# Performance work log

Measured on AMD Instinct MI355X. Metric: run time of the kernel, lower is better.

## Reference

```python
import jax, jax.numpy as jnp
import numpy as np

N_NODES = 50000
ALPHA_SLOPE = 0.2  # LeakyReLU negative slope
EPS = 1e-16


def setup_inputs() -> dict:
    key = jax.random.key(0)
    k1, k2, k3, k4 = jax.random.split(key, 4)
    in_features, heads, d = 512, 8, 32
    x = jax.random.normal(k1, (N_NODES, in_features), dtype=jnp.float32)
    edge_index = jax.random.randint(k2, (2, 800000), 0, N_NODES, dtype=jnp.int64)
    # xavier_normal with relu gain ~ sqrt(2) * sqrt(2/(fan_in+fan_out))
    w_std = np.sqrt(2.0) * np.sqrt(2.0 / (in_features + d))
    a_std = np.sqrt(2.0) * np.sqrt(2.0 / (1 + 2 * d))
    W = jax.random.normal(k3, (heads, in_features, d), dtype=jnp.float32) * w_std
    a = jax.random.normal(k4, (heads, 2 * d), dtype=jnp.float32) * a_std
    return {"x": x, "edge_index": edge_index, "W": W, "a": a}


def reference(x, edge_index, W, a):
    # x: [N, F_in], edge_index: [2, E], W: [H, F_in, D], a: [H, 2D]
    n = x.shape[0]
    d = W.shape[-1]
    e0, e1 = edge_index[0], edge_index[1]
    # per-head projected features: [N, H, D]
    h = jnp.einsum('nf,hfd->nhd', x, W)
    # attention logits: a.mm(cat(h[e0], h[e1]).T) == a_src.h[e0] + a_dst.h[e1]
    a_src, a_dst = a[:, :d], a[:, d:]          # [H, D] each
    s_src = jnp.einsum('nhd,hd->nh', h, a_src)  # [N, H]
    s_dst = jnp.einsum('nhd,hd->nh', h, a_dst)  # [N, H]
    logits = s_src[e0] + s_dst[e1]              # [E, H]
    logits = jnp.where(logits >= 0, logits, ALPHA_SLOPE * logits)  # LeakyReLU
    # segment softmax over destination node e0
    m = jax.ops.segment_max(logits, e0, num_segments=n)   # [N, H]
    ex = jnp.exp(logits - m[e0])                          # [E, H]
    denom = jax.ops.segment_sum(ex, e0, num_segments=n)   # [N, H]
    alpha = ex / (denom[e0] + EPS)                        # [E, H]
    # dropout is identity in eval mode
    # sparse aggregate: out[e0] += alpha * h[e1]
    msg = alpha[:, :, None] * h[e1]                       # [E, H, D]
    out = jax.ops.segment_sum(msg, e0, num_segments=n)    # [N, H, D]
    return out.reshape(n, -1)                             # concat heads -> [N, H*D]
```

## Files before the change

### kernel.cpp

```cpp
#include <hip/hip_runtime.h>

#define N_NODES 50000
#define N_EDGES 800000
#define IN_F    512
#define HEADS   8
#define DHEAD   32
#define NHD     256
#define SLOPE   0.2f
#define EPS_F   1e-16f
#define N_SBLK  ((N_NODES + 255) / 256)

typedef __attribute__((ext_vector_type(8))) short short8;
typedef __attribute__((ext_vector_type(4))) float f32x4;
typedef __attribute__((ext_vector_type(4))) unsigned short u16x4;

__device__ __forceinline__ unsigned short f2bf(float f) {
  unsigned int u = __float_as_uint(f);
  unsigned int r = u + 0x7FFFu + ((u >> 16) & 1u);
  return (unsigned short)(r >> 16);
}
__device__ __forceinline__ float bf2f(unsigned short s) {
  return __uint_as_float(((unsigned int)s) << 16);
}
__device__ __forceinline__ void gload_lds16(const void* g, void* l) {
  __builtin_amdgcn_global_load_lds((const __attribute__((address_space(1))) void*)g,
                                   (__attribute__((address_space(3))) void*)l, 16, 0, 0);
}

__global__ void k_cast_w(const float* __restrict__ W, unsigned short* __restrict__ WbT) {
  int id = blockIdx.x * blockDim.x + threadIdx.x;
  if (id >= NHD * IN_F) return;
  int c = id >> 9, k = id & 511;
  WbT[id] = f2bf(W[(c >> 5) * (IN_F * DHEAD) + k * DHEAD + (c & 31)]);
}

__global__ __launch_bounds__(256) void k_gemm_mfma(const float* __restrict__ x,
                                                   const unsigned short* __restrict__ WbT,
                                                   unsigned short* __restrict__ hb) {
  __shared__ unsigned short As[64 * 64];
  __shared__ unsigned short Bs[256 * 64];
  const int tid  = threadIdx.x;
  const int lane = tid & 63;
  const int wid  = tid >> 6;
  const int bm   = blockIdx.x * 64;
  const int wn   = wid * 64;

  const int arow = tid >> 3, ap = tid & 7, aq = ap ^ (arow & 7);
  const float* gA0 = x + (size_t)min(bm + arow,      N_NODES - 1) * IN_F + aq * 8;
  const float* gA1 = x + (size_t)min(bm + arow + 32, N_NODES - 1) * IN_F + aq * 8;
  unsigned short* lA0 = &As[(arow * 8 + ap) * 8];
  unsigned short* lA1 = &As[((arow + 32) * 8 + ap) * 8];

  const int bs = 512 * wid + lane;
  const int brow = bs >> 3, bp = bs & 7, bq = bp ^ (brow & 7);
  const unsigned short* gB = WbT + (size_t)brow * IN_F + bq * 8;
  unsigned short* lB = &Bs[(size_t)512 * wid * 8];

  f32x4 acc[4][4] = {};

  for (int k0 = 0; k0 < IN_F; k0 += 64) {
    __syncthreads();
#pragma unroll
    for (int it = 0; it < 8; ++it)
      gload_lds16(gB + k0 + it * 8 * IN_F, lB + it * 64 * 8);
    {
      float4 a00 = *(const float4*)(gA0 + k0);
      float4 a01 = *(const float4*)(gA0 + k0 + 4);
      float4 a10 = *(const float4*)(gA1 + k0);
      float4 a11 = *(const float4*)(gA1 + k0 + 4);
      short8 v0, v1;
      v0[0] = (short)f2bf(a00.x); v0[1] = (short)f2bf(a00.y);
      v0[2] = (short)f2bf(a00.z); v0[3] = (short)f2bf(a00.w);
      v0[4] = (short)f2bf(a01.x); v0[5] = (short)f2bf(a01.y);
      v0[6] = (short)f2bf(a01.z); v0[7] = (short)f2bf(a01.w);
      v1[0] = (short)f2bf(a10.x); v1[1] = (short)f2bf(a10.y);
      v1[2] = (short)f2bf(a10.z); v1[3] = (short)f2bf(a10.w);
      v1[4] = (short)f2bf(a11.x); v1[5] = (short)f2bf(a11.y);
      v1[6] = (short)f2bf(a11.z); v1[7] = (short)f2bf(a11.w);
      *(short8*)lA0 = v0;
      *(short8*)lA1 = v1;
    }
    __syncthreads();

#pragma unroll
    for (int kk = 0; kk < 2; ++kk) {
      short8 af[4], bfr[4];
#pragma unroll
      for (int i = 0; i < 4; ++i) {
        int r = i * 16 + (lane & 15);
        int q = kk * 4 + (lane >> 4);
        af[i] = *(const short8*)&As[(r * 8 + (q ^ (r & 7))) * 8];
      }
#pragma unroll
      for (int j = 0; j < 4; ++j) {
        int r = wn + j * 16 + (lane & 15);
        int q = kk * 4 + (lane >> 4);
        bfr[j] = *(const short8*)&Bs[(r * 8 + (q ^ (r & 7))) * 8];
      }
#pragma unroll
      for (int i = 0; i < 4; ++i)
#pragma unroll
        for (int j = 0; j < 4; ++j)
          acc[i][j] = __builtin_amdgcn_mfma_f32_16x16x32_bf16(af[i], bfr[j], acc[i][j], 0, 0, 0);
    }
  }

#pragma unroll
  for (int i = 0; i < 4; ++i) {
#pragma unroll
    for (int q = 0; q < 4; ++q) {
      int row = bm + i * 16 + (lane >> 4) * 4 + q;
      if (row < N_NODES) {
#pragma unroll
        for (int j = 0; j < 4; ++j)
          hb[(size_t)row * NHD + wn + j * 16 + (lane & 15)] = f2bf(acc[i][j][q]);
      }
    }
  }
}

__global__ __launch_bounds__(256) void k_scores(const unsigned short* __restrict__ hb,
                                                const float* __restrict__ a,
                                                float* __restrict__ s_src,
                                                float* __restrict__ s_dst) {
  int n = (blockIdx.x * blockDim.x + threadIdx.x) >> 6;
  int lane = threadIdx.x & 63;
  if (n >= N_NODES) return;
  int head = lane >> 3;
  int dofs = (lane & 7) * 4;
  u16x4 hv = *(const u16x4*)(hb + (size_t)n * NHD + lane * 4);
  float4 as = *(const float4*)(a + head * 2 * DHEAD + dofs);
  float4 ad = *(const float4*)(a + head * 2 * DHEAD + DHEAD + dofs);
  float h0 = bf2f(hv.x), h1 = bf2f(hv.y), h2 = bf2f(hv.z), h3 = bf2f(hv.w);
  float ss = h0 * as.x + h1 * as.y + h2 * as.z + h3 * as.w;
  float sd = h0 * ad.x + h1 * ad.y + h2 * ad.z + h3 * ad.w;
  ss += __shfl_xor(ss, 1); ss += __shfl_xor(ss, 2); ss += __shfl_xor(ss, 4);
  sd += __shfl_xor(sd, 1); sd += __shfl_xor(sd, 2); sd += __shfl_xor(sd, 4);
  if ((lane & 7) == 0) {
    s_src[n * 8 + head] = ss;
    s_dst[n * 8 + head] = sd;
  }
}

__global__ void k_hist(const int* __restrict__ ei, int* __restrict__ deg) {
  int e = blockIdx.x * blockDim.x + threadIdx.x;
  if (e < N_EDGES) atomicAdd(&deg[ei[e]], 1);
}

__global__ __launch_bounds__(256) void k_bsum(const int* __restrict__ deg,
                                              int* __restrict__ bsum) {
  __shared__ int sm[4];
  int i = blockIdx.x * 256 + threadIdx.x;
  int v = (i < N_NODES) ? deg[i] : 0;
#pragma unroll
  for (int o = 1; o < 64; o <<= 1) v += __shfl_xor(v, o);
  if ((threadIdx.x & 63) == 0) sm[threadIdx.x >> 6] = v;
  __syncthreads();
  if (threadIdx.x == 0) bsum[blockIdx.x] = sm[0] + sm[1] + sm[2] + sm[3];
}

__global__ __launch_bounds__(256) void k_scan_main(const int* __restrict__ deg,
                                                   const int* __restrict__ bsum,
                                                   int* __restrict__ rowptr,
                                                   int* __restrict__ cursor) {
  __shared__ int sb[256];
  __shared__ int sm[256];
  const int t = threadIdx.x;
  const int b = blockIdx.x;
  int bv = (t < N_SBLK) ? bsum[t] : 0;
  sb[t] = bv;
  int i = b * 256 + t;
  int v = (i < N_NODES) ? deg[i] : 0;
  sm[t] = v;
  __syncthreads();
#pragma unroll
  for (int o = 1; o < 256; o <<= 1) {
    int u1 = (t >= o) ? sb[t - o] : 0;
    int u2 = (t >= o) ? sm[t - o] : 0;
    __syncthreads();
    sb[t] += u1;
    sm[t] += u2;
    __syncthreads();
  }
  int boff = (b > 0) ? sb[b - 1] : 0;
  if (i < N_NODES) {
    int ex = boff + sm[t] - v;
    rowptr[i] = ex;
    cursor[i] = ex;
  }
  if (b == 0 && t == 0) rowptr[N_NODES] = sb[255];
}

__global__ void k_fill(const int* __restrict__ ei, int* __restrict__ cursor,
                       int* __restrict__ edst) {
  int e = blockIdx.x * blockDim.x + threadIdx.x;
  if (e >= N_EDGES) return;
  int p = atomicAdd(&cursor[ei[e]], 1);
  edst[p] = ei[N_EDGES + e];
}

__global__ __launch_bounds__(256) void k_aggr(const int* __restrict__ rowptr,
                                              const int* __restrict__ edst,
                                              const float* __restrict__ s_src,
                                              const float* __restrict__ s_dst,
                                              const unsigned short* __restrict__ hb,
                                              float* __restrict__ out) {
  int n = (int)((blockIdx.x * blockDim.x + threadIdx.x) >> 6);
  if (n >= N_NODES) return;
  n = __builtin_amdgcn_readfirstlane(n);
  const int lane = threadIdx.x & 63;
  const int head = lane >> 3;
  const float ssrc = s_src[n * 8 + head];
  int i = rowptr[n];
  const int iend = rowptr[n + 1];
  float den = 0.f;
  f32x4 acc = {0.f, 0.f, 0.f, 0.f};
  for (; i + 1 < iend; i += 2) {
    int d0 = edst[i], d1 = edst[i + 1];
    float v0 = ssrc + s_dst[d0 * 8 + head];
    float v1 = ssrc + s_dst[d1 * 8 + head];
    u16x4 h0 = *(const u16x4*)(hb + (size_t)d0 * NHD + lane * 4);
    u16x4 h1 = *(const u16x4*)(hb + (size_t)d1 * NHD + lane * 4);
    v0 = v0 >= 0.f ? v0 : SLOPE * v0;
    v1 = v1 >= 0.f ? v1 : SLOPE * v1;
    float e0 = __expf(v0), e1 = __expf(v1);
    den += e0 + e1;
    acc.x += e0 * bf2f(h0.x) + e1 * bf2f(h1.x);
    acc.y += e0 * bf2f(h0.y) + e1 * bf2f(h1.y);
    acc.z += e0 * bf2f(h0.z) + e1 * bf2f(h1.z);
    acc.w += e0 * bf2f(h0.w) + e1 * bf2f(h1.w);
  }
  if (i < iend) {
    int d0 = edst[i];
    float v0 = ssrc + s_dst[d0 * 8 + head];
    v0 = v0 >= 0.f ? v0 : SLOPE * v0;
    float e0 = __expf(v0);
    u16x4 h0 = *(const u16x4*)(hb + (size_t)d0 * NHD + lane * 4);
    den += e0;
    acc.x += e0 * bf2f(h0.x);
    acc.y += e0 * bf2f(h0.y);
    acc.z += e0 * bf2f(h0.z);
    acc.w += e0 * bf2f(h0.w);
  }
  float inv = 1.f / (den + EPS_F);
  *(f32x4*)(out + (size_t)n * NHD + lane * 4) = acc * inv;
}

extern "C" void kernel_launch(void* const* d_in, const int* in_sizes, int n_in,
                              void* d_out, int out_size, void* d_ws, size_t ws_size,
                              hipStream_t stream) {
  const float* x  = (const float*)d_in[0];
  const int*   ei = (const int*)d_in[1];
  const float* W  = (const float*)d_in[2];
  const float* a  = (const float*)d_in[3];
  float* out = (float*)d_out;

  unsigned short* hb  = (unsigned short*)d_ws;
  unsigned short* WbT = hb + (size_t)N_NODES * NHD;
  float* s_src = (float*)(WbT + (size_t)NHD * IN_F);
  float* s_dst = s_src + (size_t)N_NODES * HEADS;
  int* deg    = (int*)(s_dst + (size_t)N_NODES * HEADS);
  int* cursor = deg + N_NODES;
  int* rowptr = cursor + N_NODES;
  int* bsum   = rowptr + 50008;
  int* edst   = bsum + 256;

  hipMemsetAsync(deg, 0, (size_t)N_NODES * sizeof(int), stream);
  k_cast_w<<<(NHD * IN_F + 255) / 256, 256, 0, stream>>>(W, WbT);
  k_gemm_mfma<<<(N_NODES + 63) / 64, 256, 0, stream>>>(x, WbT, hb);
  k_scores<<<(N_NODES * 64 + 255) / 256, 256, 0, stream>>>(hb, a, s_src, s_dst);
  k_hist<<<(N_EDGES + 255) / 256, 256, 0, stream>>>(ei, deg);
  k_bsum<<<N_SBLK, 256, 0, stream>>>(deg, bsum);
  k_scan_main<<<N_SBLK, 256, 0, stream>>>(deg, bsum, rowptr, cursor);
  k_fill<<<(N_EDGES + 255) / 256, 256, 0, stream>>>(ei, cursor, edst);
  k_aggr<<<(N_NODES * 64 + 255) / 256, 256, 0, stream>>>(rowptr, edst, s_src, s_dst, hb, out);
}
```

Measured before the change: 204.2 us.

## Fuse score computation into GEMM, double-buffer GEMM, merge prep kernels, unroll aggregation

Attention-score dot products move into the GEMM epilogue using accumulator registers plus shuffle reductions, so the separate scores kernel and its re-read of h are removed. The GEMM gains double-buffered LDS for A and B so global loads overlap MFMA work. The weight cast and degree histogram are combined into one launch, and the aggregation loop is unrolled by four to keep more gathers in flight. LDS use per block doubles, which may lower occupancy.

```diff
diff --git a/kernel.cpp b/kernel.cpp
--- a/kernel.cpp
+++ b/kernel.cpp
@@ -27,18 +27,26 @@
                                    (__attribute__((address_space(3))) void*)l, 16, 0, 0);
 }
 
-__global__ void k_cast_w(const float* __restrict__ W, unsigned short* __restrict__ WbT) {
-  int id = blockIdx.x * blockDim.x + threadIdx.x;
-  if (id >= NHD * IN_F) return;
-  int c = id >> 9, k = id & 511;
-  WbT[id] = f2bf(W[(c >> 5) * (IN_F * DHEAD) + k * DHEAD + (c & 31)]);
+__global__ __launch_bounds__(256) void k_prep(const float* __restrict__ W,
+                                              unsigned short* __restrict__ WbT,
+                                              const int* __restrict__ ei,
+                                              int* __restrict__ deg) {
+  int id = blockIdx.x * 256 + threadIdx.x;
+  if (id < NHD * IN_F) {
+    int c = id >> 9, k = id & 511;
+    WbT[id] = f2bf(W[(c >> 5) * (IN_F * DHEAD) + k * DHEAD + (c & 31)]);
+  }
+  if (id < N_EDGES) atomicAdd(&deg[ei[id]], 1);
 }
 
 __global__ __launch_bounds__(256) void k_gemm_mfma(const float* __restrict__ x,
                                                    const unsigned short* __restrict__ WbT,
-                                                   unsigned short* __restrict__ hb) {
-  __shared__ unsigned short As[64 * 64];
-  __shared__ unsigned short Bs[256 * 64];
+                                                   unsigned short* __restrict__ hb,
+                                                   const float* __restrict__ a,
+                                                   float* __restrict__ s_src,
+                                                   float* __restrict__ s_dst) {
+  __shared__ unsigned short As[2][64 * 64];
+  __shared__ unsigned short Bs[2][256 * 64];
   const int tid  = threadIdx.x;
   const int lane = tid & 63;
   const int wid  = tid >> 6;
@@ -48,40 +56,39 @@
   const int arow = tid >> 3, ap = tid & 7, aq = ap ^ (arow & 7);
   const float* gA0 = x + (size_t)min(bm + arow,      N_NODES - 1) * IN_F + aq * 8;
   const float* gA1 = x + (size_t)min(bm + arow + 32, N_NODES - 1) * IN_F + aq * 8;
-  unsigned short* lA0 = &As[(arow * 8 + ap) * 8];
-  unsigned short* lA1 = &As[((arow + 32) * 8 + ap) * 8];
 
   const int bs = 512 * wid + lane;
   const int brow = bs >> 3, bp = bs & 7, bq = bp ^ (brow & 7);
   const unsigned short* gB = WbT + (size_t)brow * IN_F + bq * 8;
-  unsigned short* lB = &Bs[(size_t)512 * wid * 8];
 
   f32x4 acc[4][4] = {};
-
-  for (int k0 = 0; k0 < IN_F; k0 += 64) {
-    __syncthreads();
+  float4 aA[4];
+
+  auto stageB = [&](int k0, int buf) {
 #pragma unroll
     for (int it = 0; it < 8; ++it)
-      gload_lds16(gB + k0 + it * 8 * IN_F, lB + it * 64 * 8);
-    {
-      float4 a00 = *(const float4*)(gA0 + k0);
-      float4 a01 = *(const float4*)(gA0 + k0 + 4);
-      float4 a10 = *(const float4*)(gA1 + k0);
-      float4 a11 = *(const float4*)(gA1 + k0 + 4);
-      short8 v0, v1;
-      v0[0] = (short)f2bf(a00.x); v0[1] = (short)f2bf(a00.y);
-      v0[2] = (short)f2bf(a00.z); v0[3] = (short)f2bf(a00.w);
-      v0[4] = (short)f2bf(a01.x); v0[5] = (short)f2bf(a01.y);
-      v0[6] = (short)f2bf(a01.z); v0[7] = (short)f2bf(a01.w);
-      v1[0] = (short)f2bf(a10.x); v1[1] = (short)f2bf(a10.y);
-      v1[2] = (short)f2bf(a10.z); v1[3] = (short)f2bf(a10.w);
-      v1[4] = (short)f2bf(a11.x); v1[5] = (short)f2bf(a11.y);
-      v1[6] = (short)f2bf(a11.z); v1[7] = (short)f2bf(a11.w);
-      *(short8*)lA0 = v0;
-      *(short8*)lA1 = v1;
-    }
-    __syncthreads();
-
+      gload_lds16(gB + k0 + it * 8 * IN_F, &Bs[buf][(512 * wid + it * 64) * 8]);
+  };
+  auto loadA = [&](int k0) {
+    aA[0] = *(const float4*)(gA0 + k0);
+    aA[1] = *(const float4*)(gA0 + k0 + 4);
+    aA[2] = *(const float4*)(gA1 + k0);
+    aA[3] = *(const float4*)(gA1 + k0 + 4);
+  };
+  auto writeA = [&](int buf) {
+    short8 v0, v1;
+    v0[0] = (short)f2bf(aA[0].x); v0[1] = (short)f2bf(aA[0].y);
+    v0[2] = (short)f2bf(aA[0].z); v0[3] = (short)f2bf(aA[0].w);
+    v0[4] = (short)f2bf(aA[1].x); v0[5] = (short)f2bf(aA[1].y);
+    v0[6] = (short)f2bf(aA[1].z); v0[7] = (short)f2bf(aA[1].w);
+    v1[0] = (short)f2bf(aA[2].x); v1[1] = (short)f2bf(aA[2].y);
+    v1[2] = (short)f2bf(aA[2].z); v1[3] = (short)f2bf(aA[2].w);
+    v1[4] = (short)f2bf(aA[3].x); v1[5] = (short)f2bf(aA[3].y);
+    v1[6] = (short)f2bf(aA[3].z); v1[7] = (short)f2bf(aA[3].w);
+    *(short8*)&As[buf][(arow * 8 + ap) * 8] = v0;
+    *(short8*)&As[buf][((arow + 32) * 8 + ap) * 8] = v1;
+  };
+  auto compute = [&](int buf) {
 #pragma unroll
     for (int kk = 0; kk < 2; ++kk) {
       short8 af[4], bfr[4];
@@ -89,13 +96,13 @@
       for (int i = 0; i < 4; ++i) {
         int r = i * 16 + (lane & 15);
         int q = kk * 4 + (lane >> 4);
-        af[i] = *(const short8*)&As[(r * 8 + (q ^ (r & 7))) * 8];
+        af[i] = *(const short8*)&As[buf][(r * 8 + (q ^ (r & 7))) * 8];
       }
 #pragma unroll
       for (int j = 0; j < 4; ++j) {
         int r = wn + j * 16 + (lane & 15);
         int q = kk * 4 + (lane >> 4);
-        bfr[j] = *(const short8*)&Bs[(r * 8 + (q ^ (r & 7))) * 8];
+        bfr[j] = *(const short8*)&Bs[buf][(r * 8 + (q ^ (r & 7))) * 8];
       }
 #pragma unroll
       for (int i = 0; i < 4; ++i)
@@ -103,48 +110,57 @@
         for (int j = 0; j < 4; ++j)
           acc[i][j] = __builtin_amdgcn_mfma_f32_16x16x32_bf16(af[i], bfr[j], acc[i][j], 0, 0, 0);
     }
-  }
+  };
+
+  stageB(0, 0);
+  loadA(0);
+  writeA(0);
+  __syncthreads();
+
+  int cur = 0;
+#pragma unroll
+  for (int t = 0; t < 8; ++t) {
+    if (t < 7) { stageB((t + 1) * 64, cur ^ 1); loadA((t + 1) * 64); }
+    compute(cur);
+    if (t < 7) { writeA(cur ^ 1); __syncthreads(); cur ^= 1; }
+  }
+
+  const int h0 = 2 * wid, h1 = 2 * wid + 1;
+  const int dl = lane & 15;
+  const float as00 = a[h0 * 64 + dl],      as01 = a[h0 * 64 + 16 + dl];
+  const float as10 = a[h1 * 64 + dl],      as11 = a[h1 * 64 + 16 + dl];
+  const float ad00 = a[h0 * 64 + 32 + dl], ad01 = a[h0 * 64 + 48 + dl];
+  const float ad10 = a[h1 * 64 + 32 + dl], ad11 = a[h1 * 64 + 48 + dl];
 
 #pragma unroll
   for (int i = 0; i < 4; ++i) {
 #pragma unroll
     for (int q = 0; q < 4; ++q) {
       int row = bm + i * 16 + (lane >> 4) * 4 + q;
+      float ss0 = acc[i][0][q] * as00 + acc[i][1][q] * as01;
+      float ss1 = acc[i][2][q] * as10 + acc[i][3][q] * as11;
+      float sd0 = acc[i][0][q] * ad00 + acc[i][1][q] * ad01;
+      float sd1 = acc[i][2][q] * ad10 + acc[i][3][q] * ad11;
+#pragma unroll
+      for (int o = 1; o < 16; o <<= 1) {
+        ss0 += __shfl_xor(ss0, o);
+        ss1 += __shfl_xor(ss1, o);
+        sd0 += __shfl_xor(sd0, o);
+        sd1 += __shfl_xor(sd1, o);
+      }
       if (row < N_NODES) {
 #pragma unroll
         for (int j = 0; j < 4; ++j)
-          hb[(size_t)row * NHD + wn + j * 16 + (lane & 15)] = f2bf(acc[i][j][q]);
+          hb[(size_t)row * NHD + wn + j * 16 + dl] = f2bf(acc[i][j][q]);
+        if (dl == 0) {
+          s_src[row * 8 + h0] = ss0;
+          s_src[row * 8 + h1] = ss1;
+          s_dst[row * 8 + h0] = sd0;
+          s_dst[row * 8 + h1] = sd1;
+        }
       }
     }
   }
-}
-
-__global__ __launch_bounds__(256) void k_scores(const unsigned short* __restrict__ hb,
-                                                const float* __restrict__ a,
-                                                float* __restrict__ s_src,
-                                                float* __restrict__ s_dst) {
-  int n = (blockIdx.x * blockDim.x + threadIdx.x) >> 6;
-  int lane = threadIdx.x & 63;
-  if (n >= N_NODES) return;
-  int head = lane >> 3;
-  int dofs = (lane & 7) * 4;
-  u16x4 hv = *(const u16x4*)(hb + (size_t)n * NHD + lane * 4);
-  float4 as = *(const float4*)(a + head * 2 * DHEAD + dofs);
-  float4 ad = *(const float4*)(a + head * 2 * DHEAD + DHEAD + dofs);
-  float h0 = bf2f(hv.x), h1 = bf2f(hv.y), h2 = bf2f(hv.z), h3 = bf2f(hv.w);
-  float ss = h0 * as.x + h1 * as.y + h2 * as.z + h3 * as.w;
-  float sd = h0 * ad.x + h1 * ad.y + h2 * ad.z + h3 * ad.w;
-  ss += __shfl_xor(ss, 1); ss += __shfl_xor(ss, 2); ss += __shfl_xor(ss, 4);
-  sd += __shfl_xor(sd, 1); sd += __shfl_xor(sd, 2); sd += __shfl_xor(sd, 4);
-  if ((lane & 7) == 0) {
-    s_src[n * 8 + head] = ss;
-    s_dst[n * 8 + head] = sd;
-  }
-}
-
-__global__ void k_hist(const int* __restrict__ ei, int* __restrict__ deg) {
-  int e = blockIdx.x * blockDim.x + threadIdx.x;
-  if (e < N_EDGES) atomicAdd(&deg[ei[e]], 1);
 }
 
 __global__ __launch_bounds__(256) void k_bsum(const int* __restrict__ deg,
@@ -215,32 +231,38 @@
   const int iend = rowptr[n + 1];
   float den = 0.f;
   f32x4 acc = {0.f, 0.f, 0.f, 0.f};
-  for (; i + 1 < iend; i += 2) {
-    int d0 = edst[i], d1 = edst[i + 1];
+  for (; i + 3 < iend; i += 4) {
+    int d0 = edst[i], d1 = edst[i + 1], d2 = edst[i + 2], d3 = edst[i + 3];
     float v0 = ssrc + s_dst[d0 * 8 + head];
     float v1 = ssrc + s_dst[d1 * 8 + head];
-    u16x4 h0 = *(const u16x4*)(hb + (size_t)d0 * NHD + lane * 4);
-    u16x4 h1 = *(const u16x4*)(hb + (size_t)d1 * NHD + lane * 4);
+    float v2 = ssrc + s_dst[d2 * 8 + head];
+    float v3 = ssrc + s_dst[d3 * 8 + head];
+    u16x4 g0 = *(const u16x4*)(hb + (size_t)d0 * NHD + lane * 4);
+    u16x4 g1 = *(const u16x4*)(hb + (size_t)d1 * NHD + lane * 4);
+    u16x4 g2 = *(const u16x4*)(hb + (size_t)d2 * NHD + lane * 4);
+    u16x4 g3 = *(const u16x4*)(hb + (size_t)d3 * NHD + lane * 4);
     v0 = v0 >= 0.f ? v0 : SLOPE * v0;
     v1 = v1 >= 0.f ? v1 : SLOPE * v1;
-    float e0 = __expf(v0), e1 = __expf(v1);
-    den += e0 + e1;
-    acc.x += e0 * bf2f(h0.x) + e1 * bf2f(h1.x);
-    acc.y += e0 * bf2f(h0.y) + e1 * bf2f(h1.y);
-    acc.z += e0 * bf2f(h0.z) + e1 * bf2f(h1.z);
-    acc.w += e0 * bf2f(h0.w) + e1 * bf2f(h1.w);
-  }
-  if (i < iend) {
+    v2 = v2 >= 0.f ? v2 : SLOPE * v2;
+    v3 = v3 >= 0.f ? v3 : SLOPE * v3;
+    float e0 = __expf(v0), e1 = __expf(v1), e2 = __expf(v2), e3 = __expf(v3);
+    den += (e0 + e1) + (e2 + e3);
+    acc.x += e0 * bf2f(g0.x) + e1 * bf2f(g1.x) + e2 * bf2f(g2.x) + e3 * bf2f(g3.x);
+    acc.y += e0 * bf2f(g0.y) + e1 * bf2f(g1.y) + e2 * bf2f(g2.y) + e3 * bf2f(g3.y);
+    acc.z += e0 * bf2f(g0.z) + e1 * bf2f(g1.z) + e2 * bf2f(g2.z) + e3 * bf2f(g3.z);
+    acc.w += e0 * bf2f(g0.w) + e1 * bf2f(g1.w) + e2 * bf2f(g2.w) + e3 * bf2f(g3.w);
+  }
+  for (; i < iend; ++i) {
     int d0 = edst[i];
     float v0 = ssrc + s_dst[d0 * 8 + head];
     v0 = v0 >= 0.f ? v0 : SLOPE * v0;
     float e0 = __expf(v0);
-    u16x4 h0 = *(const u16x4*)(hb + (size_t)d0 * NHD + lane * 4);
+    u16x4 g0 = *(const u16x4*)(hb + (size_t)d0 * NHD + lane * 4);
     den += e0;
-    acc.x += e0 * bf2f(h0.x);
-    acc.y += e0 * bf2f(h0.y);
-    acc.z += e0 * bf2f(h0.z);
-    acc.w += e0 * bf2f(h0.w);
+    acc.x += e0 * bf2f(g0.x);
+    acc.y += e0 * bf2f(g0.y);
+    acc.z += e0 * bf2f(g0.z);
+    acc.w += e0 * bf2f(g0.w);
   }
   float inv = 1.f / (den + EPS_F);
   *(f32x4*)(out + (size_t)n * NHD + lane * 4) = acc * inv;
@@ -266,10 +288,8 @@
   int* edst   = bsum + 256;
 
   hipMemsetAsync(deg, 0, (size_t)N_NODES * sizeof(int), stream);
-  k_cast_w<<<(NHD * IN_F + 255) / 256, 256, 0, stream>>>(W, WbT);
-  k_gemm_mfma<<<(N_NODES + 63) / 64, 256, 0, stream>>>(x, WbT, hb);
-  k_scores<<<(N_NODES * 64 + 255) / 256, 256, 0, stream>>>(hb, a, s_src, s_dst);
-  k_hist<<<(N_EDGES + 255) / 256, 256, 0, stream>>>(ei, deg);
+  k_prep<<<(N_EDGES + 255) / 256, 256, 0, stream>>>(W, WbT, ei, deg);
+  k_gemm_mfma<<<(N_NODES + 63) / 64, 256, 0, stream>>>(x, WbT, hb, a, s_src, s_dst);
   k_bsum<<<N_SBLK, 256, 0, stream>>>(deg, bsum);
   k_scan_main<<<N_SBLK, 256, 0, stream>>>(deg, bsum, rowptr, cursor);
   k_fill<<<(N_EDGES + 255) / 256, 256, 0, stream>>>(ei, cursor, edst);
```

Result: slower. 212.1 us (+3.9%).
